# Performance work log

Hardware: AMD Instinct MI355X
Metric: run time of the kernel (lower is better)

Reference implementation:

```python
import jax, jax.numpy as jnp
import numpy as np

B, T, C, HS = 8, 2048, 768, 256  # batch, seq(block_size), n_embed, head_size


def setup_inputs() -> dict:
    key = jax.random.key(0)
    kx, kq, kk, kv = jax.random.split(key, 4)
    scale = 1.0 / np.sqrt(C)
    return {
        "x": jax.random.normal(kx, (B, T, C), dtype=jnp.float32),
        # torch nn.Linear(n_embed, head_size, bias=False) computes x @ W.T;
        # store weights pre-transposed as [in, out].
        "Wq": jax.random.normal(kq, (C, HS), dtype=jnp.float32) * scale,
        "Wk": jax.random.normal(kk, (C, HS), dtype=jnp.float32) * scale,
        "Wv": jax.random.normal(kv, (C, HS), dtype=jnp.float32) * scale,
    }


def reference(x, Wq, Wk, Wv):
    Bx, Tx, Cx = x.shape
    q = x @ Wq  # [B,T,HS]
    k = x @ Wk  # [B,T,HS]
    v = x @ Wv  # [B,T,HS]
    # NOTE: original scales by C**-0.5 with C = n_embed (not head_size)
    att = jnp.einsum('btd,bsd->bts', q, k) * (Cx ** -0.5)  # [B,T,T]
    causal = jnp.tril(jnp.ones((Tx, Tx), dtype=bool))
    att = jnp.where(causal, att, -jnp.inf)
    probs = jax.nn.softmax(att, axis=-1)
    # dropout=0.0 -> identity (eval mode)
    out = jnp.einsum('bts,bsd->btd', probs, v)  # [B,T,HS]
    return out
```

## Files before the change

kernel.cpp:

```cpp
#include <hip/hip_runtime.h>
#include <hip/hip_bf16.h>
#include <math.h>

#define B_  8
#define T_  2048
#define C_  768
#define HS_ 256

#define CHUNK_TILES 8
#define CHUNKS_PER_BATCH 80
#define NPART (CHUNKS_PER_BATCH * B_)

typedef float  f32x4  __attribute__((ext_vector_type(4)));
typedef __bf16 bf16x8 __attribute__((ext_vector_type(8)));
typedef __bf16 bf16x4 __attribute__((ext_vector_type(4)));

#define MFMA16(a, b, c) __builtin_amdgcn_mfma_f32_16x16x32_bf16((a), (b), (c), 0, 0, 0)

#define GLOAD_LDS16(gp, lp)                                                     \
    __builtin_amdgcn_global_load_lds(                                           \
        (const __attribute__((address_space(1))) void*)(gp),                    \
        (__attribute__((address_space(3))) void*)(lp), 16, 0, 0)

__device__ __forceinline__ int chunk_cum(int q) {
    int g = q >> 3;
    return 4 * g * (g + 1) + (q - 8 * g) * (g + 1);
}

__global__ __launch_bounds__(256) void xb_kernel(const float* __restrict__ x,
                                                 __bf16* __restrict__ xb) {
    size_t i = ((size_t)blockIdx.x * 256 + threadIdx.x) * 8;
    f32x4 a = *(const f32x4*)(x + i);
    f32x4 b = *(const f32x4*)(x + i + 4);
    bf16x8 o;
    o[0] = (__bf16)a[0]; o[1] = (__bf16)a[1]; o[2] = (__bf16)a[2]; o[3] = (__bf16)a[3];
    o[4] = (__bf16)b[0]; o[5] = (__bf16)b[1]; o[6] = (__bf16)b[2]; o[7] = (__bf16)b[3];
    *(bf16x8*)(xb + i) = o;
}

__global__ __launch_bounds__(256) void wt_kernel(const float* __restrict__ Wq,
                                                 const float* __restrict__ Wk,
                                                 const float* __restrict__ Wv,
                                                 __bf16* __restrict__ wt_all,
                                                 float qscale) {
    int idx = blockIdx.x * 256 + threadIdx.x;
    int mat = blockIdx.y;
    const float* W = (mat == 0) ? Wq : ((mat == 1) ? Wk : Wv);
    float scale = (mat == 0) ? qscale : 1.0f;
    int k = idx >> 8;
    int n = idx & 255;
    wt_all[((size_t)mat * HS_ + n) * C_ + k] = (__bf16)(W[idx] * scale);
}

__global__ __launch_bounds__(256) void proj_kernel(const __bf16* __restrict__ xb,
                                                   const __bf16* __restrict__ wt,
                                                   __bf16* __restrict__ qf_,
                                                   __bf16* __restrict__ kf_,
                                                   __bf16* __restrict__ vf_) {
    __shared__ alignas(16) __bf16 ldsA[128 * 32];
    __shared__ alignas(16) __bf16 ldsB[128 * 32];

    const int tid  = threadIdx.x;
    const int w    = tid >> 6;
    const int lane = tid & 63;
    const int cm   = lane & 15;
    const int quad = lane >> 4;
    const int wm   = w & 1;
    const int wn   = w >> 1;
    const int m0   = blockIdx.x * 128;
    const int n0   = blockIdx.y * 128;

    f32x4 acc[4][4];
#pragma unroll
    for (int i = 0; i < 4; i++)
#pragma unroll
        for (int j = 0; j < 4; j++) acc[i][j] = (f32x4){0.f, 0.f, 0.f, 0.f};

    for (int k0 = 0; k0 < C_; k0 += 32) {
        __syncthreads();
#pragma unroll
        for (int h = 0; h < 2; h++) {
            int c = tid + h * 256;
            GLOAD_LDS16(xb + (size_t)(m0 + (c >> 2)) * C_ + k0 + (c & 3) * 8,
                        ldsA + c * 8);
        }
#pragma unroll
        for (int h = 0; h < 2; h++) {
            int c = tid + h * 256;
            GLOAD_LDS16(wt + (size_t)(n0 + (c >> 2)) * C_ + k0 + (c & 3) * 8,
                        ldsB + c * 8);
        }
        __syncthreads();

        bf16x8 af[4], bfr[4];
#pragma unroll
        for (int mt = 0; mt < 4; mt++)
            af[mt] = *(const bf16x8*)&ldsA[(wm * 64 + mt * 16 + cm) * 32 + quad * 8];
#pragma unroll
        for (int nt = 0; nt < 4; nt++)
            bfr[nt] = *(const bf16x8*)&ldsB[(wn * 64 + nt * 16 + cm) * 32 + quad * 8];
#pragma unroll
        for (int mt = 0; mt < 4; mt++)
#pragma unroll
            for (int nt = 0; nt < 4; nt++)
                acc[mt][nt] = MFMA16(af[mt], bfr[nt], acc[mt][nt]);
    }

    const int mat   = n0 >> 8;
    const int dBase = (n0 & 255) + wn * 64;
    const int b     = m0 >> 11;
    const int rt    = ((m0 & 2047) + wm * 64) >> 6;

    if (mat == 0) {
#pragma unroll
        for (int mt = 0; mt < 4; mt++)
#pragma unroll
            for (int nt = 0; nt < 4; nt++) {
                int ksq   = (dBase >> 5) + (nt >> 1);
                int quad2 = (nt & 1) * 2 + (cm >> 3);
                int j     = cm & 7;
                size_t base = ((((size_t)(b * 32 + rt) * 4 + mt) * 8 + ksq) * 64
                               + quad2 * 16) * 8 + j;
#pragma unroll
                for (int i = 0; i < 4; i++)
                    qf_[base + (quad * 4 + i) * 8] = (__bf16)acc[mt][nt][i];
            }
    } else if (mat == 1) {
#pragma unroll
        for (int mt = 0; mt < 4; mt++)
#pragma unroll
            for (int nt = 0; nt < 4; nt++) {
                int ksq   = (dBase >> 5) + (nt >> 1);
                int quad2 = (nt & 1) * 2 + (cm >> 3);
                int j     = cm & 7;
                size_t base = ((((size_t)(b * 32 + rt) * 8 + ksq) * 4 + mt) * 64
                               + quad2 * 16) * 8 + j;
#pragma unroll
                for (int i = 0; i < 4; i++)
                    kf_[base + (quad * 4 + i) * 8] = (__bf16)acc[mt][nt][i];
            }
    } else {
#pragma unroll
        for (int mt = 0; mt < 4; mt++) {
            int ks2   = (mt >> 1) & 1;
            int quadF = (mt & 1) * 2 + (quad >> 1);
            int jb    = (quad & 1) * 4;
#pragma unroll
            for (int nt = 0; nt < 4; nt++) {
                int ntv = (dBase >> 4) + nt;
                size_t idx = ((((size_t)(b * 32 + rt) * 2 + ks2) * 16 + ntv) * 64
                              + quadF * 16 + cm) * 8 + jb;
                bf16x4 v4;
                v4[0] = (__bf16)acc[mt][nt][0]; v4[1] = (__bf16)acc[mt][nt][1];
                v4[2] = (__bf16)acc[mt][nt][2]; v4[3] = (__bf16)acc[mt][nt][3];
                *(bf16x4*)(vf_ + idx) = v4;
            }
        }
    }
}

__global__ __launch_bounds__(256) void flash_part(const __bf16* __restrict__ qf_,
                                                  const __bf16* __restrict__ kf_,
                                                  const __bf16* __restrict__ vf_,
                                                  float* __restrict__ Opart,
                                                  float* __restrict__ mpart,
                                                  float* __restrict__ lpart) {
    __shared__ alignas(16) __bf16 ldsK[8 * 4 * 64 * 8];
    __shared__ alignas(16) __bf16 ldsV[2 * 16 * 64 * 8];

    const int tid  = threadIdx.x;
    const int w    = tid >> 6;
    const int lane = tid & 63;
    const int cm   = lane & 15;
    const int quad = lane >> 4;

    const int pid = blockIdx.x;
    const int b   = pid & 7;
    int r = (CHUNKS_PER_BATCH - 1) - (pid >> 3);
    int qblk = 0, ci = 0;
    {
        int rr = r;
#pragma unroll
        for (int g = 0; g < 4; g++) {
            int gs = 8 * (g + 1);
            if (rr < gs) { qblk = g * 8 + rr / (g + 1); ci = rr % (g + 1); break; }
            rr -= gs;
        }
    }
    const int lpid = b * CHUNKS_PER_BATCH + r;
    const int kt_begin = ci * CHUNK_TILES;
    const int kt_end   = min(kt_begin + CHUNK_TILES, qblk + 1);

    const __bf16* qp = qf_ + (((size_t)(b * 32 + qblk) * 4 + w) * 8) * 512 + lane * 8;
    bf16x8 qf[8];
#pragma unroll
    for (int ks = 0; ks < 8; ks++) qf[ks] = *(const bf16x8*)(qp + ks * 512);

    f32x4 accO[16];
#pragma unroll
    for (int i = 0; i < 16; i++) accO[i] = (f32x4){0.f, 0.f, 0.f, 0.f};
    float mi[4], li[4];
#pragma unroll
    for (int i = 0; i < 4; i++) { mi[i] = -__builtin_inff(); li[i] = 0.f; }

    const int qg = qblk * 64 + w * 16 + quad * 4;

    for (int kt = kt_begin; kt < kt_end; kt++) {
        __syncthreads();

        const __bf16* kg = kf_ + ((size_t)(b * 32 + kt) * 8) * 2048;
        const __bf16* vg = vf_ + ((size_t)(b * 32 + kt) * 2) * 8192;
#pragma unroll
        for (int h = 0; h < 8; h++) {
            GLOAD_LDS16(kg + (h * 256 + tid) * 8, ldsK + (h * 256 + w * 64) * 8);
            GLOAD_LDS16(vg + (h * 256 + tid) * 8, ldsV + (h * 256 + w * 64) * 8);
        }
        __syncthreads();

        f32x4 s[4];
#pragma unroll
        for (int i = 0; i < 4; i++) s[i] = (f32x4){0.f, 0.f, 0.f, 0.f};
#pragma unroll
        for (int nsub = 0; nsub < 4; nsub++) {
#pragma unroll
            for (int ks = 0; ks < 8; ks++) {
                bf16x8 kfr = *(const bf16x8*)&ldsK[ks * 2048 + nsub * 512 + lane * 8];
                s[nsub] = MFMA16(qf[ks], kfr, s[nsub]);
            }
        }
        if (kt == qblk) {
#pragma unroll
            for (int nsub = 0; nsub < 4; nsub++)
#pragma unroll
                for (int i = 0; i < 4; i++)
                    if (kt * 64 + nsub * 16 + cm > qg + i)
                        s[nsub][i] = -__builtin_inff();
        }
        float pm[4];
#pragma unroll
        for (int i = 0; i < 4; i++)
            pm[i] = fmaxf(fmaxf(s[0][i], s[1][i]), fmaxf(s[2][i], s[3][i]));
#pragma unroll
        for (int off = 1; off < 16; off <<= 1)
#pragma unroll
            for (int i = 0; i < 4; i++)
                pm[i] = fmaxf(pm[i], __shfl_xor(pm[i], off));

        float alpha[4], rs[4], p[4][4];
#pragma unroll
        for (int i = 0; i < 4; i++) {
            float mn = fmaxf(mi[i], pm[i]);
            alpha[i] = exp2f(mi[i] - mn);
            mi[i] = mn;
            rs[i] = 0.f;
        }
#pragma unroll
        for (int nsub = 0; nsub < 4; nsub++)
#pragma unroll
            for (int i = 0; i < 4; i++) {
                p[nsub][i] = exp2f(s[nsub][i] - mi[i]);
                rs[i] += p[nsub][i];
            }
#pragma unroll
        for (int off = 1; off < 16; off <<= 1)
#pragma unroll
            for (int i = 0; i < 4; i++)
                rs[i] += __shfl_xor(rs[i], off);
#pragma unroll
        for (int i = 0; i < 4; i++) li[i] = li[i] * alpha[i] + rs[i];
#pragma unroll
        for (int nt = 0; nt < 16; nt++)
#pragma unroll
            for (int i = 0; i < 4; i++) accO[nt][i] *= alpha[i];

        __syncthreads();

        __bf16* ldsP = ldsK + w * 1024;
#pragma unroll
        for (int nsub = 0; nsub < 4; nsub++)
#pragma unroll
            for (int i = 0; i < 4; i++) {
                int c = nsub * 16 + cm;
                ldsP[(c >> 5) * 512 + ((c >> 3) & 3) * 128 + (quad * 4 + i) * 8 + (c & 7)]
                    = (__bf16)p[nsub][i];
            }
#pragma unroll
        for (int ks2 = 0; ks2 < 2; ks2++) {
            bf16x8 pf = *(const bf16x8*)&ldsP[ks2 * 512 + quad * 128 + cm * 8];
#pragma unroll
            for (int nt = 0; nt < 16; nt++) {
                bf16x8 vfr = *(const bf16x8*)&ldsV[ks2 * 8192 + nt * 512 + lane * 8];
                accO[nt] = MFMA16(pf, vfr, accO[nt]);
            }
        }
    }

    const int rloc = w * 16 + quad * 4;
    float* op = Opart + ((size_t)lpid * 64 + rloc) * HS_;
#pragma unroll
    for (int nt = 0; nt < 16; nt++)
#pragma unroll
        for (int i = 0; i < 4; i++)
            op[(size_t)i * HS_ + nt * 16 + cm] = accO[nt][i];
    if (cm == 0) {
#pragma unroll
        for (int i = 0; i < 4; i++) {
            mpart[lpid * 64 + rloc + i] = mi[i];
            lpart[lpid * 64 + rloc + i] = li[i];
        }
    }
}

__global__ __launch_bounds__(256) void flash_combine(const float* __restrict__ Opart,
                                                     const float* __restrict__ mpart,
                                                     const float* __restrict__ lpart,
                                                     float* __restrict__ out) {
    const int b    = blockIdx.x >> 5;
    const int qblk = blockIdx.x & 31;
    const int nc   = (qblk >> 3) + 1;
    const int pid0 = b * CHUNKS_PER_BATCH + chunk_cum(qblk);

    const int tid  = threadIdx.x;
    const int col  = (tid & 63) * 4;
    const int r0   = blockIdx.y * 16 + (tid >> 6) * 4;

    for (int rr = 0; rr < 4; rr++) {
        const int row = r0 + rr;
        float ms = -__builtin_inff();
        for (int c = 0; c < nc; c++)
            ms = fmaxf(ms, mpart[(pid0 + c) * 64 + row]);
        f32x4 acc = (f32x4){0.f, 0.f, 0.f, 0.f};
        float l = 0.f;
        for (int c = 0; c < nc; c++) {
            float sc = exp2f(mpart[(pid0 + c) * 64 + row] - ms);
            l += lpart[(pid0 + c) * 64 + row] * sc;
            f32x4 o = *(const f32x4*)(Opart + ((size_t)(pid0 + c) * 64 + row) * HS_ + col);
            acc[0] += o[0] * sc; acc[1] += o[1] * sc;
            acc[2] += o[2] * sc; acc[3] += o[3] * sc;
        }
        float inv = 1.0f / l;
        f32x4 res = (f32x4){acc[0] * inv, acc[1] * inv, acc[2] * inv, acc[3] * inv};
        *(f32x4*)(out + ((size_t)(b * T_ + qblk * 64 + row)) * HS_ + col) = res;
    }
}

extern "C" void kernel_launch(void* const* d_in, const int* in_sizes, int n_in,
                              void* d_out, int out_size, void* d_ws, size_t ws_size,
                              hipStream_t stream) {
    const float* x  = (const float*)d_in[0];
    const float* Wq = (const float*)d_in[1];
    const float* Wk = (const float*)d_in[2];
    const float* Wv = (const float*)d_in[3];
    float* out = (float*)d_out;

    char* ws = (char*)d_ws;
    size_t off = 0;
    __bf16* wt_all = (__bf16*)(ws + off); off += 1179648;
    __bf16* qfrag  = (__bf16*)(ws + off); off += 8388608;
    __bf16* kfrag  = (__bf16*)(ws + off); off += 8388608;
    __bf16* vfrag  = (__bf16*)(ws + off); off += 8388608;
    __bf16* xb     = (__bf16*)(ws + off);
    float*  Opart  = (float*)(ws + off);  off += (size_t)NPART * 64 * HS_ * 4;
    float*  mpart  = (float*)(ws + off);  off += (size_t)NPART * 64 * 4;
    float*  lpart  = (float*)(ws + off);

    float qscale = 1.4426950408889634f / sqrtf((float)C_);

    xb_kernel<<<dim3(6144), 256, 0, stream>>>(x, xb);
    wt_kernel<<<dim3(768, 3), 256, 0, stream>>>(Wq, Wk, Wv, wt_all, qscale);
    proj_kernel<<<dim3(128, 6), 256, 0, stream>>>(xb, wt_all, qfrag, kfrag, vfrag);
    flash_part<<<dim3(NPART), 256, 0, stream>>>(qfrag, kfrag, vfrag, Opart, mpart, lpart);
    flash_combine<<<dim3(256, 4), 256, 0, stream>>>(Opart, mpart, lpart, out);
}
```

Baseline: 200.6 us.

## Use 128-row query blocks with 512-thread workgroups and bf16 partial outputs

The flash-attention partial kernel moves from 64-row query blocks to 128-row blocks with 8 waves, so each K/V tile loaded into LDS is reused by twice as many query rows. Chunks are now 4 key tiles, which changes the split-K schedule and partition count. Partial O outputs are stored as bf16 instead of fp32 to halve the write and read traffic in the combine kernel. In exchange, the precision of the partials drops, and the larger blocks with more register pressure may lower occupancy. The causal mask check is now per wave.

Result: slower. 242.5 us (+20.9%).

```diff
diff --git a/kernel.cpp b/kernel.cpp
--- a/kernel.cpp
+++ b/kernel.cpp
@@ -7,8 +7,8 @@
 #define C_  768
 #define HS_ 256
 
-#define CHUNK_TILES 8
-#define CHUNKS_PER_BATCH 80
+#define CHUNK_TILES 4
+#define CHUNKS_PER_BATCH 72
 #define NPART (CHUNKS_PER_BATCH * B_)
 
 typedef float  f32x4  __attribute__((ext_vector_type(4)));
@@ -22,9 +22,9 @@
         (const __attribute__((address_space(1))) void*)(gp),                    \
         (__attribute__((address_space(3))) void*)(lp), 16, 0, 0)
 
-__device__ __forceinline__ int chunk_cum(int q) {
-    int g = q >> 3;
-    return 4 * g * (g + 1) + (q - 8 * g) * (g + 1);
+__device__ __forceinline__ int chunk_cum128(int qb) {
+    int p = qb >> 1;
+    return p * (p + 1) + (qb & 1) * (p + 1);
 }
 
 __global__ __launch_bounds__(256) void xb_kernel(const float* __restrict__ x,
@@ -159,12 +159,12 @@
     }
 }
 
-__global__ __launch_bounds__(256) void flash_part(const __bf16* __restrict__ qf_,
-                                                  const __bf16* __restrict__ kf_,
-                                                  const __bf16* __restrict__ vf_,
-                                                  float* __restrict__ Opart,
-                                                  float* __restrict__ mpart,
-                                                  float* __restrict__ lpart) {
+__global__ __launch_bounds__(512, 4) void flash_part(const __bf16* __restrict__ qf_,
+                                                     const __bf16* __restrict__ kf_,
+                                                     const __bf16* __restrict__ vf_,
+                                                     __bf16* __restrict__ Opart,
+                                                     float* __restrict__ mpart,
+                                                     float* __restrict__ lpart) {
     __shared__ alignas(16) __bf16 ldsK[8 * 4 * 64 * 8];
     __shared__ alignas(16) __bf16 ldsV[2 * 16 * 64 * 8];
 
@@ -176,22 +176,22 @@
 
     const int pid = blockIdx.x;
     const int b   = pid & 7;
-    int r = (CHUNKS_PER_BATCH - 1) - (pid >> 3);
-    int qblk = 0, ci = 0;
+    const int r   = (CHUNKS_PER_BATCH - 1) - (pid >> 3);
+    int qb = 0, ci = 0;
     {
         int rr = r;
-#pragma unroll
-        for (int g = 0; g < 4; g++) {
-            int gs = 8 * (g + 1);
-            if (rr < gs) { qblk = g * 8 + rr / (g + 1); ci = rr % (g + 1); break; }
-            rr -= gs;
+        for (int j = 0; j < 16; j++) {
+            int c = (j >> 1) + 1;
+            if (rr < c) { qb = j; ci = rr; break; }
+            rr -= c;
         }
     }
     const int lpid = b * CHUNKS_PER_BATCH + r;
     const int kt_begin = ci * CHUNK_TILES;
-    const int kt_end   = min(kt_begin + CHUNK_TILES, qblk + 1);
-
-    const __bf16* qp = qf_ + (((size_t)(b * 32 + qblk) * 4 + w) * 8) * 512 + lane * 8;
+    const int kt_end   = min(kt_begin + CHUNK_TILES, 2 * qb + 2);
+
+    const int qt = 2 * qb + (w >> 2);
+    const __bf16* qp = qf_ + (((size_t)(b * 32 + qt) * 4 + (w & 3)) * 8) * 512 + lane * 8;
     bf16x8 qf[8];
 #pragma unroll
     for (int ks = 0; ks < 8; ks++) qf[ks] = *(const bf16x8*)(qp + ks * 512);
@@ -203,7 +203,8 @@
 #pragma unroll
     for (int i = 0; i < 4; i++) { mi[i] = -__builtin_inff(); li[i] = 0.f; }
 
-    const int qg = qblk * 64 + w * 16 + quad * 4;
+    const int wrow = qb * 128 + w * 16;
+    const int qg   = wrow + quad * 4;
 
     for (int kt = kt_begin; kt < kt_end; kt++) {
         __syncthreads();
@@ -211,9 +212,9 @@
         const __bf16* kg = kf_ + ((size_t)(b * 32 + kt) * 8) * 2048;
         const __bf16* vg = vf_ + ((size_t)(b * 32 + kt) * 2) * 8192;
 #pragma unroll
-        for (int h = 0; h < 8; h++) {
-            GLOAD_LDS16(kg + (h * 256 + tid) * 8, ldsK + (h * 256 + w * 64) * 8);
-            GLOAD_LDS16(vg + (h * 256 + tid) * 8, ldsV + (h * 256 + w * 64) * 8);
+        for (int h = 0; h < 4; h++) {
+            GLOAD_LDS16(kg + (size_t)(h * 512 + tid) * 8, ldsK + (h * 512 + w * 64) * 8);
+            GLOAD_LDS16(vg + (size_t)(h * 512 + tid) * 8, ldsV + (h * 512 + w * 64) * 8);
         }
         __syncthreads();
 
@@ -228,7 +229,7 @@
                 s[nsub] = MFMA16(qf[ks], kfr, s[nsub]);
             }
         }
-        if (kt == qblk) {
+        if (kt * 64 + 63 > wrow) {
 #pragma unroll
             for (int nsub = 0; nsub < 4; nsub++)
 #pragma unroll
@@ -296,29 +297,29 @@
     }
 
     const int rloc = w * 16 + quad * 4;
-    float* op = Opart + ((size_t)lpid * 64 + rloc) * HS_;
+    __bf16* op = Opart + ((size_t)lpid * 128 + rloc) * HS_;
 #pragma unroll
     for (int nt = 0; nt < 16; nt++)
 #pragma unroll
         for (int i = 0; i < 4; i++)
-            op[(size_t)i * HS_ + nt * 16 + cm] = accO[nt][i];
+            op[(size_t)i * HS_ + nt * 16 + cm] = (__bf16)accO[nt][i];
     if (cm == 0) {
 #pragma unroll
         for (int i = 0; i < 4; i++) {
-            mpart[lpid * 64 + rloc + i] = mi[i];
-            lpart[lpid * 64 + rloc + i] = li[i];
-        }
-    }
-}
-
-__global__ __launch_bounds__(256) void flash_combine(const float* __restrict__ Opart,
+            mpart[lpid * 128 + rloc + i] = mi[i];
+            lpart[lpid * 128 + rloc + i] = li[i];
+        }
+    }
+}
+
+__global__ __launch_bounds__(256) void flash_combine(const __bf16* __restrict__ Opart,
                                                      const float* __restrict__ mpart,
                                                      const float* __restrict__ lpart,
                                                      float* __restrict__ out) {
-    const int b    = blockIdx.x >> 5;
-    const int qblk = blockIdx.x & 31;
-    const int nc   = (qblk >> 3) + 1;
-    const int pid0 = b * CHUNKS_PER_BATCH + chunk_cum(qblk);
+    const int b    = blockIdx.x >> 4;
+    const int qb   = blockIdx.x & 15;
+    const int nc   = (qb >> 1) + 1;
+    const int pid0 = b * CHUNKS_PER_BATCH + chunk_cum128(qb);
 
     const int tid  = threadIdx.x;
     const int col  = (tid & 63) * 4;
@@ -328,19 +329,19 @@
         const int row = r0 + rr;
         float ms = -__builtin_inff();
         for (int c = 0; c < nc; c++)
-            ms = fmaxf(ms, mpart[(pid0 + c) * 64 + row]);
+            ms = fmaxf(ms, mpart[(pid0 + c) * 128 + row]);
         f32x4 acc = (f32x4){0.f, 0.f, 0.f, 0.f};
         float l = 0.f;
         for (int c = 0; c < nc; c++) {
-            float sc = exp2f(mpart[(pid0 + c) * 64 + row] - ms);
-            l += lpart[(pid0 + c) * 64 + row] * sc;
-            f32x4 o = *(const f32x4*)(Opart + ((size_t)(pid0 + c) * 64 + row) * HS_ + col);
-            acc[0] += o[0] * sc; acc[1] += o[1] * sc;
-            acc[2] += o[2] * sc; acc[3] += o[3] * sc;
+            float sc = exp2f(mpart[(pid0 + c) * 128 + row] - ms);
+            l += lpart[(pid0 + c) * 128 + row] * sc;
+            bf16x4 o = *(const bf16x4*)(Opart + ((size_t)(pid0 + c) * 128 + row) * HS_ + col);
+            acc[0] += (float)o[0] * sc; acc[1] += (float)o[1] * sc;
+            acc[2] += (float)o[2] * sc; acc[3] += (float)o[3] * sc;
         }
         float inv = 1.0f / l;
         f32x4 res = (f32x4){acc[0] * inv, acc[1] * inv, acc[2] * inv, acc[3] * inv};
-        *(f32x4*)(out + ((size_t)(b * T_ + qblk * 64 + row)) * HS_ + col) = res;
+        *(f32x4*)(out + ((size_t)(b * T_ + qb * 128 + row)) * HS_ + col) = res;
     }
 }
 
@@ -360,8 +361,8 @@
     __bf16* kfrag  = (__bf16*)(ws + off); off += 8388608;
     __bf16* vfrag  = (__bf16*)(ws + off); off += 8388608;
     __bf16* xb     = (__bf16*)(ws + off);
-    float*  Opart  = (float*)(ws + off);  off += (size_t)NPART * 64 * HS_ * 4;
-    float*  mpart  = (float*)(ws + off);  off += (size_t)NPART * 64 * 4;
+    __bf16* Opart  = (__bf16*)(ws + off); off += (size_t)NPART * 128 * HS_ * 2;
+    float*  mpart  = (float*)(ws + off);  off += (size_t)NPART * 128 * 4;
     float*  lpart  = (float*)(ws + off);
 
     float qscale = 1.4426950408889634f / sqrtf((float)C_);
@@ -369,6 +370,6 @@
     xb_kernel<<<dim3(6144), 256, 0, stream>>>(x, xb);
     wt_kernel<<<dim3(768, 3), 256, 0, stream>>>(Wq, Wk, Wv, wt_all, qscale);
     proj_kernel<<<dim3(128, 6), 256, 0, stream>>>(xb, wt_all, qfrag, kfrag, vfrag);
-    flash_part<<<dim3(NPART), 256, 0, stream>>>(qfrag, kfrag, vfrag, Opart, mpart, lpart);
-    flash_combine<<<dim3(256, 4), 256, 0, stream>>>(Opart, mpart, lpart, out);
-}
+    flash_part<<<dim3(NPART), 512, 0, stream>>>(qfrag, kfrag, vfrag, Opart, mpart, lpart);
+    flash_combine<<<dim3(128, 8), 256, 0, stream>>>(Opart, mpart, lpart, out);
+}
```
